# Optimization experiments

Hardware: AMD Instinct MI355X
Metric: run time of the kernel (lower is better)

The kernel has to match this reference:

```python
import jax, jax.numpy as jnp
import numpy as np
import math

B, T, D, H, E = 4, 2048, 1024, 4096, 8
CAPACITY_FACTOR = 1.0
MIN_CAPACITY = 4
Z_LOSS_COEF = 0.001
AUX_LOSS_COEF = 0.01


def setup_inputs() -> dict:
    key = jax.random.key(0)
    ks = jax.random.split(key, 5)
    x = jax.random.normal(ks[0], (B, T, D), jnp.float32)
    Wg = jax.random.normal(ks[1], (D, E), jnp.float32) * 0.02
    W1 = jax.random.normal(ks[2], (E, D, H), jnp.float32) * (1.0 / math.sqrt(D))
    b1 = jnp.zeros((E, H), jnp.float32)
    W2 = jax.random.normal(ks[3], (E, H, D), jnp.float32) * (1.0 / math.sqrt(H))
    b2 = jnp.zeros((E, D), jnp.float32)
    return {"x": x, "Wg": Wg, "W1": W1, "b1": b1, "W2": W2, "b2": b2}


def reference(x, Wg, W1, b1, W2, b2):
    b, t, d = x.shape
    e = Wg.shape[1]
    N = b * t
    capacity = max(MIN_CAPACITY, math.ceil(CAPACITY_FACTOR * N / e))  # static
    xf = x.reshape(N, d)

    # ---- Router (top-1, z-loss + aux load-balancing loss) ----
    logits = xf @ Wg                                   # [N, E]
    probs = jax.nn.softmax(logits, axis=-1)
    z_loss = jnp.mean(jax.nn.logsumexp(logits, axis=-1) ** 2)
    expert_index = jnp.argmax(logits, axis=-1)         # [N]
    expert_prob = jnp.take_along_axis(probs, expert_index[:, None], axis=1)[:, 0]
    counts = jax.ops.segment_sum(jnp.ones((N,), jnp.float32), expert_index,
                                 num_segments=e)       # bincount
    f_i = counts / N
    p_i = probs.mean(axis=0)
    aux_loss = AUX_LOSS_COEF * e * jnp.sum(f_i * p_i) + Z_LOSS_COEF * z_loss

    # ---- Sort-based dispatch ----
    sort_idx = jnp.argsort(expert_index)               # stable sort by expert
    se = expert_index[sort_idx]                        # sorted expert ids
    xs = xf[sort_idx]                                  # tokens in sorted order
    ps = expert_prob[sort_idx]                         # probs in sorted order
    counts_i = counts.astype(jnp.int32)
    start = jnp.cumsum(counts_i) - counts_i            # per-expert start offsets
    pos = jnp.arange(N, dtype=jnp.int32) - start[se]   # slot within expert
    keep = pos < capacity                              # capacity drop
    slot = jnp.where(keep, pos, capacity)              # overflow -> trash slot

    # Gather tokens into per-expert capacity buffer [E, capacity+1, D]
    buf = jnp.zeros((e, capacity + 1, d), xf.dtype).at[se, slot].set(xs)

    # ---- Batched per-expert MLP (grouped GEMM) ----
    h = jax.nn.gelu(jnp.einsum('ecd,edh->ech', buf, W1) + b1[:, None, :],
                    approximate=False)
    o = jnp.einsum('ech,ehd->ecd', h, W2) + b2[:, None, :]

    # ---- Combine: gather back, zero dropped tokens, unsort ----
    out_sorted = jnp.where(keep[:, None], o[se, slot], jnp.zeros((), o.dtype))
    out = jnp.zeros_like(xf).at[sort_idx].set(out_sorted)
    # NOTE: faithful to original code, which multiplies the UNSORTED output by
    # the SORTED probabilities (prob_sorted), a quirk of the source module.
    out = out * ps[:, None]
    return out.reshape(b, t, d), aux_loss
```

## Files before the change

kernel.cpp:

```cpp
#include <hip/hip_runtime.h>
#include <math.h>

#define N_TOK 8192
#define DIM   1024
#define NEXP  8
#define HID   4096
#define CAP   1024
#define TPT   (N_TOK / 256)
#define RT_BLOCKS 1024
#define RT_TPB 8

typedef _Float16 f16x8 __attribute__((ext_vector_type(8)));
typedef _Float16 f16x4 __attribute__((ext_vector_type(4)));
typedef float    f32x4 __attribute__((ext_vector_type(4)));

__device__ __forceinline__ float gelu_fast(float v) {
    const float v2 = v * v;
    const float u = v * (0.79788456f + 0.035677408136f * v2);
    const float ex = __expf(2.f * u);
    const float th = 1.f - 2.f / (1.f + ex);
    return 0.5f * v * (1.f + th);
}

__device__ __forceinline__ void gl_lds16(const void* g, void* l) {
    __builtin_amdgcn_global_load_lds(
        (const __attribute__((address_space(1))) unsigned int*)g,
        (__attribute__((address_space(3))) unsigned int*)l, 16, 0, 0);
}

__global__ __launch_bounds__(256) void router_kernel(
    const float* __restrict__ x, const float* __restrict__ Wg,
    int* __restrict__ ei, float* __restrict__ eprob,
    float* __restrict__ pp)
{
    __shared__ float psum_s[NEXP + 1];
    const int tid = threadIdx.x;
    const int w = tid >> 6, lane = tid & 63;
    if (tid <= NEXP) psum_s[tid] = 0.f;
    __syncthreads();

    float p_loc[NEXP];
#pragma unroll
    for (int e = 0; e < NEXP; ++e) p_loc[e] = 0.f;
    float z_loc = 0.f;

#pragma unroll
    for (int ti = 0; ti < 2; ++ti) {
        const int t = blockIdx.x * RT_TPB + w * 2 + ti;
        const float* xr = x + (size_t)t * DIM;
        float acc[NEXP];
#pragma unroll
        for (int e = 0; e < NEXP; ++e) acc[e] = 0.f;
#pragma unroll
        for (int k = 0; k < DIM / 256; ++k) {
            const int d = k * 256 + lane * 4;
            const float4 xv = *(const float4*)(xr + d);
            const float xs[4] = {xv.x, xv.y, xv.z, xv.w};
#pragma unroll
            for (int u = 0; u < 4; ++u) {
                const float4 w0 = *(const float4*)(Wg + (size_t)(d + u) * NEXP);
                const float4 w1 = *(const float4*)(Wg + (size_t)(d + u) * NEXP + 4);
                acc[0] += xs[u] * w0.x; acc[1] += xs[u] * w0.y;
                acc[2] += xs[u] * w0.z; acc[3] += xs[u] * w0.w;
                acc[4] += xs[u] * w1.x; acc[5] += xs[u] * w1.y;
                acc[6] += xs[u] * w1.z; acc[7] += xs[u] * w1.w;
            }
        }
#pragma unroll
        for (int off = 32; off > 0; off >>= 1) {
#pragma unroll
            for (int e = 0; e < NEXP; ++e)
                acc[e] += __shfl_down(acc[e], off, 64);
        }
        if (lane == 0) {
            float m = acc[0]; int arg = 0;
#pragma unroll
            for (int e = 1; e < NEXP; ++e) { if (acc[e] > m) { m = acc[e]; arg = e; } }
            float ex[NEXP]; float se = 0.f;
#pragma unroll
            for (int e = 0; e < NEXP; ++e) { ex[e] = expf(acc[e] - m); se += ex[e]; }
            const float lse = m + logf(se);
            const float inv = 1.f / se;
#pragma unroll
            for (int e = 0; e < NEXP; ++e) p_loc[e] += ex[e] * inv;
            z_loc += lse * lse;
            ei[t] = arg;
            eprob[t] = ex[arg] * inv;
        }
    }
    if (lane == 0) {
#pragma unroll
        for (int e = 0; e < NEXP; ++e) atomicAdd(&psum_s[e], p_loc[e]);
        atomicAdd(&psum_s[NEXP], z_loc);
    }
    __syncthreads();
    if (tid <= NEXP) pp[blockIdx.x * (NEXP + 1) + tid] = psum_s[tid];
}

__global__ __launch_bounds__(256) void dispatch_kernel(
    const int* __restrict__ ei, const float* __restrict__ eprob,
    int* __restrict__ slot_to_token, int* __restrict__ sort_idx,
    float* __restrict__ scale,
    const float* __restrict__ pp,
    int* __restrict__ dropped, int* __restrict__ n_dropped,
    float* __restrict__ aux_out)
{
    __shared__ int hist[NEXP][256];
    __shared__ int start_s[NEXP];
    __shared__ float red_s[4][NEXP + 1];
    __shared__ float tot_s[NEXP + 1];
    __shared__ int ndrop_s;
    const int t = threadIdx.x;
    const int w = t >> 6, lane = t & 63;
    if (t == 0) ndrop_s = 0;

    {
        float v[NEXP + 1];
#pragma unroll
        for (int j = 0; j <= NEXP; ++j) v[j] = 0.f;
        for (int g = 0; g < RT_BLOCKS / 256; ++g)
#pragma unroll
            for (int j = 0; j <= NEXP; ++j) v[j] += pp[(size_t)(g * 256 + t) * (NEXP + 1) + j];
#pragma unroll
        for (int j = 0; j <= NEXP; ++j) {
            float s = v[j];
#pragma unroll
            for (int off = 32; off > 0; off >>= 1) s += __shfl_down(s, off, 64);
            if (lane == 0) red_s[w][j] = s;
        }
    }
    __syncthreads();
    if (t <= NEXP) tot_s[t] = red_s[0][t] + red_s[1][t] + red_s[2][t] + red_s[3][t];
    __syncthreads();

    int le[TPT];
    int lh[NEXP];
#pragma unroll
    for (int e = 0; e < NEXP; ++e) lh[e] = 0;
    const int base = t * TPT;
    for (int i = 0; i < TPT; ++i) {
        const int e = ei[base + i];
        le[i] = e;
        lh[e]++;
    }
#pragma unroll
    for (int e = 0; e < NEXP; ++e) hist[e][t] = lh[e];
    __syncthreads();
    for (int off = 1; off < 256; off <<= 1) {
        int v[NEXP];
#pragma unroll
        for (int e = 0; e < NEXP; ++e) v[e] = (t >= off) ? hist[e][t - off] : 0;
        __syncthreads();
#pragma unroll
        for (int e = 0; e < NEXP; ++e) hist[e][t] += v[e];
        __syncthreads();
    }
    if (t == 0) {
        int s = 0;
        for (int e = 0; e < NEXP; ++e) { start_s[e] = s; s += hist[e][255]; }
    }
    __syncthreads();
    int run[NEXP];
#pragma unroll
    for (int e = 0; e < NEXP; ++e) run[e] = (t > 0) ? hist[e][t - 1] : 0;
    for (int i = 0; i < TPT; ++i) {
        const int n = base + i;
        const int e = le[i];
        const int pos = run[e]++;
        sort_idx[start_s[e] + pos] = n;
        if (pos < CAP) {
            slot_to_token[e * CAP + pos] = n;
        } else {
            const int di = atomicAdd(&ndrop_s, 1);
            dropped[di] = n;
        }
    }
    __syncthreads();
    for (int n = t; n < N_TOK; n += 256) scale[n] = eprob[sort_idx[n]];
    if (t == 0) {
        n_dropped[0] = ndrop_s;
        float s = 0.f;
        for (int e = 0; e < NEXP; ++e) {
            const float f = (float)hist[e][255] / (float)N_TOK;
            const float p = tot_s[e] / (float)N_TOK;
            s += f * p;
        }
        aux_out[0] = 0.01f * (float)NEXP * s + 0.001f * (tot_s[NEXP] / (float)N_TOK);
    }
}

__global__ __launch_bounds__(256) void zero_dropped_kernel(
    const int* __restrict__ dropped, const int* __restrict__ n_dropped,
    float* __restrict__ out)
{
    const int nd = n_dropped[0];
    const float4 z = make_float4(0.f, 0.f, 0.f, 0.f);
    for (int idx = blockIdx.x; idx < nd; idx += gridDim.x) {
        const int tok = dropped[idx];
        *(float4*)(out + (size_t)tok * DIM + threadIdx.x * 4) = z;
    }
}

__global__ __launch_bounds__(256) void gather_kernel(
    const float* __restrict__ x, const int* __restrict__ slot_to_token,
    _Float16* __restrict__ Xbuf)
{
    const int slot = blockIdx.x;
    const int tok = slot_to_token[slot];
    const int c = threadIdx.x * 4;
    float4 v = make_float4(0.f, 0.f, 0.f, 0.f);
    if (tok >= 0) v = *(const float4*)(x + (size_t)tok * DIM + c);
    f16x4 o;
    o[0] = (_Float16)v.x; o[1] = (_Float16)v.y;
    o[2] = (_Float16)v.z; o[3] = (_Float16)v.w;
    *(f16x4*)(Xbuf + (size_t)slot * DIM + c) = o;
}

template<int R, int C>
__global__ __launch_bounds__(256) void transpose_f32_f16(
    const float* __restrict__ in, _Float16* __restrict__ outT)
{
    const int e = blockIdx.z;
    const int r0 = blockIdx.y * 64, c0 = blockIdx.x * 64;
    const float* pin = in + (size_t)e * R * C;
    _Float16* pot = outT + (size_t)e * R * C;
    __shared__ _Float16 tile[64][72];
    const int tid = threadIdx.x;
    const int rr = tid >> 4, cc = (tid & 15) * 4;
#pragma unroll
    for (int ri = 0; ri < 4; ++ri) {
        const int row = rr + ri * 16;
        const float4 v = *(const float4*)&pin[(size_t)(r0 + row) * C + c0 + cc];
        tile[cc + 0][row] = (_Float16)v.x;
        tile[cc + 1][row] = (_Float16)v.y;
        tile[cc + 2][row] = (_Float16)v.z;
        tile[cc + 3][row] = (_Float16)v.w;
    }
    __syncthreads();
    const int c = tid >> 2, rs = (tid & 3) * 16;
    const f16x8 o0 = *(const f16x8*)&tile[c][rs];
    const f16x8 o1 = *(const f16x8*)&tile[c][rs + 8];
    _Float16* po = &pot[(size_t)(c0 + c) * R + r0 + rs];
    *(f16x8*)po = o0;
    *(f16x8*)(po + 8) = o1;
}

__global__ __launch_bounds__(256) void gemm1_kernel(
    const _Float16* __restrict__ A, const _Float16* __restrict__ Bt,
    const float* __restrict__ b1, _Float16* __restrict__ Hbuf)
{
    const int b = blockIdx.x;
    const int xcd = b & 7, q = b >> 3;
    const int nb = (xcd << 2) | (q & 3);
    const int mb = q >> 2;
    const int e  = mb >> 3;
    const _Float16* Ab = A  + (size_t)mb * 128 * DIM;
    const _Float16* Bb = Bt + (size_t)e * HID * DIM + (size_t)nb * 128 * DIM;
    __shared__ _Float16 As[128 * 64];
    __shared__ _Float16 Bs[128 * 64];
    const int tid = threadIdx.x;
    const int lane = tid & 63, w = tid >> 6;
    const int wm = (w >> 1) * 64, wn = (w & 1) * 64;
    const int lr = lane & 15, quad = lane >> 4;

    f32x4 acc[4][4];
#pragma unroll
    for (int i = 0; i < 4; ++i)
#pragma unroll
        for (int j = 0; j < 4; ++j) acc[i][j] = (f32x4)0.f;

    for (int k0 = 0; k0 < DIM; k0 += 64) {
#pragma unroll
        for (int i = 0; i < 4; ++i) {
            const int idx = i * 256 + tid;
            const int row = idx >> 3, s = idx & 7;
            const int seg = s ^ (row & 7);
            gl_lds16(Ab + (size_t)row * DIM + k0 + seg * 8, &As[idx * 8]);
            gl_lds16(Bb + (size_t)row * DIM + k0 + seg * 8, &Bs[idx * 8]);
        }
        __syncthreads();
#pragma unroll
        for (int kk = 0; kk < 2; ++kk) {
            f16x8 af[4], bf[4];
#pragma unroll
            for (int i = 0; i < 4; ++i) {
                const int R = wm + i * 16 + lr;
                af[i] = *(const f16x8*)&As[R * 64 + (((kk << 2) | quad) ^ (R & 7)) * 8];
            }
#pragma unroll
            for (int j = 0; j < 4; ++j) {
                const int R = wn + j * 16 + lr;
                bf[j] = *(const f16x8*)&Bs[R * 64 + (((kk << 2) | quad) ^ (R & 7)) * 8];
            }
#pragma unroll
            for (int i = 0; i < 4; ++i)
#pragma unroll
                for (int j = 0; j < 4; ++j)
                    acc[i][j] = __builtin_amdgcn_mfma_f32_16x16x32_f16(af[i], bf[j], acc[i][j], 0, 0, 0);
        }
        __syncthreads();
    }
    float bias[4];
#pragma unroll
    for (int j = 0; j < 4; ++j)
        bias[j] = b1[(size_t)e * HID + (size_t)nb * 128 + wn + j * 16 + lr];
#pragma unroll
    for (int i = 0; i < 4; ++i) {
#pragma unroll
        for (int r = 0; r < 4; ++r) {
            const size_t row = (size_t)mb * 128 + wm + i * 16 + quad * 4 + r;
            _Float16* hr = Hbuf + row * HID + (size_t)nb * 128;
#pragma unroll
            for (int j = 0; j < 4; ++j)
                hr[wn + j * 16 + lr] = (_Float16)gelu_fast(acc[i][j][r] + bias[j]);
        }
    }
}

__global__ __launch_bounds__(256) void gemm2_kernel(
    const _Float16* __restrict__ A, const _Float16* __restrict__ Bt,
    const float* __restrict__ b2, const int* __restrict__ slot_to_token,
    const float* __restrict__ scale, float* __restrict__ out)
{
    const int b = blockIdx.x;
    const int xcd = b & 7, q = b >> 3;
    const int nb = (xcd << 1) | (q & 1);
    const int mb = q >> 1;
    const int e  = mb >> 3;
    const _Float16* Ab = A  + (size_t)mb * 128 * HID;
    const _Float16* Bb = Bt + (size_t)e * DIM * HID + (size_t)nb * 64 * HID;
    __shared__ _Float16 As[128 * 64];
    __shared__ _Float16 Bs[64 * 64];
    const int tid = threadIdx.x;
    const int lane = tid & 63, w = tid >> 6;
    const int wm = (w >> 1) * 64, wn = (w & 1) * 32;
    const int lr = lane & 15, quad = lane >> 4;

    f32x4 acc[4][2];
#pragma unroll
    for (int i = 0; i < 4; ++i)
#pragma unroll
        for (int j = 0; j < 2; ++j) acc[i][j] = (f32x4)0.f;

    for (int k0 = 0; k0 < HID; k0 += 64) {
#pragma unroll
        for (int i = 0; i < 4; ++i) {
            const int idx = i * 256 + tid;
            const int row = idx >> 3, s = idx & 7;
            const int seg = s ^ (row & 7);
            gl_lds16(Ab + (size_t)row * HID + k0 + seg * 8, &As[idx * 8]);
        }
#pragma unroll
        for (int i = 0; i < 2; ++i) {
            const int idx = i * 256 + tid;
            const int row = idx >> 3, s = idx & 7;
            const int seg = s ^ (row & 7);
            gl_lds16(Bb + (size_t)row * HID + k0 + seg * 8, &Bs[idx * 8]);
        }
        __syncthreads();
#pragma unroll
        for (int kk = 0; kk < 2; ++kk) {
            f16x8 af[4], bf[2];
#pragma unroll
            for (int i = 0; i < 4; ++i) {
                const int R = wm + i * 16 + lr;
                af[i] = *(const f16x8*)&As[R * 64 + (((kk << 2) | quad) ^ (R & 7)) * 8];
            }
#pragma unroll
            for (int j = 0; j < 2; ++j) {
                const int R = wn + j * 16 + lr;
                bf[j] = *(const f16x8*)&Bs[R * 64 + (((kk << 2) | quad) ^ (R & 7)) * 8];
            }
#pragma unroll
            for (int i = 0; i < 4; ++i)
#pragma unroll
                for (int j = 0; j < 2; ++j)
                    acc[i][j] = __builtin_amdgcn_mfma_f32_16x16x32_f16(af[i], bf[j], acc[i][j], 0, 0, 0);
        }
        __syncthreads();
    }
    float bias[2];
#pragma unroll
    for (int j = 0; j < 2; ++j)
        bias[j] = b2[(size_t)e * DIM + (size_t)nb * 64 + wn + j * 16 + lr];
#pragma unroll
    for (int i = 0; i < 4; ++i) {
#pragma unroll
        for (int r = 0; r < 4; ++r) {
            const int slot = mb * 128 + wm + i * 16 + quad * 4 + r;
            const int tok = slot_to_token[slot];
            if (tok >= 0) {
                const float sc = scale[tok];
                float* orow = out + (size_t)tok * DIM + (size_t)nb * 64;
#pragma unroll
                for (int j = 0; j < 2; ++j)
                    orow[wn + j * 16 + lr] = (acc[i][j][r] + bias[j]) * sc;
            }
        }
    }
}

extern "C" void kernel_launch(void* const* d_in, const int* in_sizes, int n_in,
                              void* d_out, int out_size, void* d_ws, size_t ws_size,
                              hipStream_t stream)
{
    const float* x  = (const float*)d_in[0];
    const float* Wg = (const float*)d_in[1];
    const float* W1 = (const float*)d_in[2];
    const float* b1 = (const float*)d_in[3];
    const float* W2 = (const float*)d_in[4];
    const float* b2 = (const float*)d_in[5];
    float* out = (float*)d_out;

    _Float16* Wt   = (_Float16*)d_ws;
    _Float16* Xbuf = Wt + (size_t)NEXP * HID * DIM;
    _Float16* Hbuf = Xbuf + (size_t)N_TOK * DIM;
    int*   ei    = (int*)(Hbuf + (size_t)N_TOK * HID);
    float* eprob = (float*)(ei + N_TOK);
    int*   sort_idx = (int*)(eprob + N_TOK);
    float* scale = (float*)(sort_idx + N_TOK);
    int*   s2t   = (int*)(scale + N_TOK);
    float* pp    = (float*)(s2t + NEXP * CAP);
    int*   dropped = (int*)(pp + RT_BLOCKS * (NEXP + 1));
    int*   n_dropped = dropped + N_TOK;

    hipMemsetAsync(s2t, 0xFF, (size_t)NEXP * CAP * sizeof(int), stream);

    transpose_f32_f16<DIM, HID><<<dim3(HID / 64, DIM / 64, NEXP), 256, 0, stream>>>(W1, Wt);
    router_kernel<<<RT_BLOCKS, 256, 0, stream>>>(x, Wg, ei, eprob, pp);
    dispatch_kernel<<<1, 256, 0, stream>>>(ei, eprob, s2t, sort_idx, scale,
                                           pp, dropped, n_dropped,
                                           out + (size_t)N_TOK * DIM);
    zero_dropped_kernel<<<128, 256, 0, stream>>>(dropped, n_dropped, out);
    gather_kernel<<<NEXP * CAP, 256, 0, stream>>>(x, s2t, Xbuf);
    gemm1_kernel<<<2048, 256, 0, stream>>>(Xbuf, Wt, b1, Hbuf);
    transpose_f32_f16<HID, DIM><<<dim3(DIM / 64, HID / 64, NEXP), 256, 0, stream>>>(W2, Wt);
    gemm2_kernel<<<1024, 256, 0, stream>>>(Hbuf, Wt, b2, s2t, scale, out);
}
```

Measured before the change: 597.7 us.

## Double-buffer expert GEMMs with 256-row tiles, 512-thread blocks and XCD-aligned experts

Both grouped GEMM kernels move to 512-thread blocks with larger tiles: 256x256 for the first GEMM and 256x128 for the second. Each uses double-buffered LDS so the next K-tile loads while MFMAs run on the current one, split into four phases with raised wave priority around the MFMA bursts. Blocks are mapped so each XCD handles one expert's weights, which should improve L2 reuse of the weight tiles. The larger LDS footprint and register use reduce occupancy, and the grid shrinks to 512 and 256 blocks, which may leave tail imbalance across CUs.

```diff
diff --git a/kernel.cpp b/kernel.cpp
--- a/kernel.cpp
+++ b/kernel.cpp
@@ -245,156 +245,217 @@
     *(f16x8*)(po + 8) = o1;
 }
 
-__global__ __launch_bounds__(256) void gemm1_kernel(
+
+__global__ __launch_bounds__(512, 2) void gemm1_kernel(
     const _Float16* __restrict__ A, const _Float16* __restrict__ Bt,
     const float* __restrict__ b1, _Float16* __restrict__ Hbuf)
 {
     const int b = blockIdx.x;
     const int xcd = b & 7, q = b >> 3;
-    const int nb = (xcd << 2) | (q & 3);
-    const int mb = q >> 2;
-    const int e  = mb >> 3;
-    const _Float16* Ab = A  + (size_t)mb * 128 * DIM;
-    const _Float16* Bb = Bt + (size_t)e * HID * DIM + (size_t)nb * 128 * DIM;
-    __shared__ _Float16 As[128 * 64];
-    __shared__ _Float16 Bs[128 * 64];
+    const int mb = (xcd << 2) | (q & 3);
+    const int nb = q >> 2;
+    const int e  = xcd;
+    const _Float16* Ab = A  + (size_t)mb * 256 * DIM;
+    const _Float16* Bb = Bt + (size_t)e * HID * DIM + (size_t)nb * 256 * DIM;
+    __shared__ _Float16 As[2][256 * 64];
+    __shared__ _Float16 Bs[2][256 * 64];
     const int tid = threadIdx.x;
     const int lane = tid & 63, w = tid >> 6;
-    const int wm = (w >> 1) * 64, wn = (w & 1) * 64;
+    const int wr = w >> 2, wc = w & 3;
     const int lr = lane & 15, quad = lane >> 4;
-
-    f32x4 acc[4][4];
-#pragma unroll
-    for (int i = 0; i < 4; ++i)
-#pragma unroll
-        for (int j = 0; j < 4; ++j) acc[i][j] = (f32x4)0.f;
-
-    for (int k0 = 0; k0 < DIM; k0 += 64) {
+    const int rb = wr * 128, cb = wc * 64;
+
+    auto stageA = [&](int t, int buf) {
 #pragma unroll
         for (int i = 0; i < 4; ++i) {
-            const int idx = i * 256 + tid;
+            const int idx = i * 512 + tid;
             const int row = idx >> 3, s = idx & 7;
             const int seg = s ^ (row & 7);
-            gl_lds16(Ab + (size_t)row * DIM + k0 + seg * 8, &As[idx * 8]);
-            gl_lds16(Bb + (size_t)row * DIM + k0 + seg * 8, &Bs[idx * 8]);
-        }
-        __syncthreads();
-#pragma unroll
-        for (int kk = 0; kk < 2; ++kk) {
-            f16x8 af[4], bf[4];
-#pragma unroll
-            for (int i = 0; i < 4; ++i) {
-                const int R = wm + i * 16 + lr;
-                af[i] = *(const f16x8*)&As[R * 64 + (((kk << 2) | quad) ^ (R & 7)) * 8];
-            }
-#pragma unroll
-            for (int j = 0; j < 4; ++j) {
-                const int R = wn + j * 16 + lr;
-                bf[j] = *(const f16x8*)&Bs[R * 64 + (((kk << 2) | quad) ^ (R & 7)) * 8];
-            }
-#pragma unroll
-            for (int i = 0; i < 4; ++i)
-#pragma unroll
-                for (int j = 0; j < 4; ++j)
-                    acc[i][j] = __builtin_amdgcn_mfma_f32_16x16x32_f16(af[i], bf[j], acc[i][j], 0, 0, 0);
-        }
-        __syncthreads();
-    }
+            gl_lds16(Ab + (size_t)row * DIM + t * 64 + seg * 8, &As[buf][idx * 8]);
+        }
+    };
+    auto stageB = [&](int t, int buf) {
+#pragma unroll
+        for (int i = 0; i < 4; ++i) {
+            const int idx = i * 512 + tid;
+            const int row = idx >> 3, s = idx & 7;
+            const int seg = s ^ (row & 7);
+            gl_lds16(Bb + (size_t)row * DIM + t * 64 + seg * 8, &Bs[buf][idx * 8]);
+        }
+    };
+
+    f32x4 acc[8][4];
+#pragma unroll
+    for (int i = 0; i < 8; ++i)
+#pragma unroll
+        for (int j = 0; j < 4; ++j) acc[i][j] = (f32x4)0.f;
+
+    stageA(0, 0);
+    stageB(0, 0);
+    const int NT = DIM / 64;
+#pragma unroll 2
+    for (int t = 0; t < NT; ++t) {
+        const int cur = t & 1, nxt = cur ^ 1;
+        asm volatile("s_waitcnt vmcnt(0)" ::: "memory");
+        __builtin_amdgcn_s_barrier();
+#pragma unroll
+        for (int ph = 0; ph < 4; ++ph) {
+            if (ph == 0 && t + 1 < NT) stageA(t + 1, nxt);
+            if (ph == 1 && t + 1 < NT) stageB(t + 1, nxt);
+            const int mih = (ph >> 1) * 4, njh = (ph & 1) * 2;
+            f16x8 af[4][2], bf[2][2];
+#pragma unroll
+            for (int mi = 0; mi < 4; ++mi)
+#pragma unroll
+                for (int kk = 0; kk < 2; ++kk) {
+                    const int R = rb + (mih + mi) * 16 + lr;
+                    af[mi][kk] = *(const f16x8*)&As[cur][R * 64 + (((kk << 2) | quad) ^ (R & 7)) * 8];
+                }
+#pragma unroll
+            for (int nj = 0; nj < 2; ++nj)
+#pragma unroll
+                for (int kk = 0; kk < 2; ++kk) {
+                    const int R = cb + (njh + nj) * 16 + lr;
+                    bf[nj][kk] = *(const f16x8*)&Bs[cur][R * 64 + (((kk << 2) | quad) ^ (R & 7)) * 8];
+                }
+            __builtin_amdgcn_s_barrier();
+            __builtin_amdgcn_s_setprio(1);
+#pragma unroll
+            for (int kk = 0; kk < 2; ++kk)
+#pragma unroll
+                for (int mi = 0; mi < 4; ++mi)
+#pragma unroll
+                    for (int nj = 0; nj < 2; ++nj)
+                        acc[mih + mi][njh + nj] = __builtin_amdgcn_mfma_f32_16x16x32_f16(
+                            af[mi][kk], bf[nj][kk], acc[mih + mi][njh + nj], 0, 0, 0);
+            __builtin_amdgcn_s_setprio(0);
+            if (ph < 3) __builtin_amdgcn_s_barrier();
+        }
+    }
+
+    const int colb = nb * 256 + cb;
     float bias[4];
 #pragma unroll
-    for (int j = 0; j < 4; ++j)
-        bias[j] = b1[(size_t)e * HID + (size_t)nb * 128 + wn + j * 16 + lr];
-#pragma unroll
-    for (int i = 0; i < 4; ++i) {
+    for (int nj = 0; nj < 4; ++nj)
+        bias[nj] = b1[(size_t)e * HID + colb + nj * 16 + lr];
+#pragma unroll
+    for (int mi = 0; mi < 8; ++mi) {
 #pragma unroll
         for (int r = 0; r < 4; ++r) {
-            const size_t row = (size_t)mb * 128 + wm + i * 16 + quad * 4 + r;
-            _Float16* hr = Hbuf + row * HID + (size_t)nb * 128;
-#pragma unroll
-            for (int j = 0; j < 4; ++j)
-                hr[wn + j * 16 + lr] = (_Float16)gelu_fast(acc[i][j][r] + bias[j]);
-        }
-    }
-}
-
-__global__ __launch_bounds__(256) void gemm2_kernel(
+            const size_t row = (size_t)mb * 256 + rb + mi * 16 + quad * 4 + r;
+            _Float16* hr = Hbuf + row * HID + colb;
+#pragma unroll
+            for (int nj = 0; nj < 4; ++nj)
+                hr[nj * 16 + lr] = (_Float16)gelu_fast(acc[mi][nj][r] + bias[nj]);
+        }
+    }
+}
+
+__global__ __launch_bounds__(512, 2) void gemm2_kernel(
     const _Float16* __restrict__ A, const _Float16* __restrict__ Bt,
     const float* __restrict__ b2, const int* __restrict__ slot_to_token,
     const float* __restrict__ scale, float* __restrict__ out)
 {
     const int b = blockIdx.x;
     const int xcd = b & 7, q = b >> 3;
-    const int nb = (xcd << 1) | (q & 1);
-    const int mb = q >> 1;
-    const int e  = mb >> 3;
-    const _Float16* Ab = A  + (size_t)mb * 128 * HID;
-    const _Float16* Bb = Bt + (size_t)e * DIM * HID + (size_t)nb * 64 * HID;
-    __shared__ _Float16 As[128 * 64];
-    __shared__ _Float16 Bs[64 * 64];
+    const int mb = (xcd << 2) | (q & 3);
+    const int nb = q >> 2;
+    const int e  = xcd;
+    const _Float16* Ab = A  + (size_t)mb * 256 * HID;
+    const _Float16* Bb = Bt + (size_t)e * DIM * HID + (size_t)nb * 128 * HID;
+    __shared__ _Float16 As[2][256 * 64];
+    __shared__ _Float16 Bs[2][128 * 64];
     const int tid = threadIdx.x;
     const int lane = tid & 63, w = tid >> 6;
-    const int wm = (w >> 1) * 64, wn = (w & 1) * 32;
+    const int wr = w >> 1, wc = w & 1;
     const int lr = lane & 15, quad = lane >> 4;
-
-    f32x4 acc[4][2];
-#pragma unroll
-    for (int i = 0; i < 4; ++i)
-#pragma unroll
-        for (int j = 0; j < 2; ++j) acc[i][j] = (f32x4)0.f;
-
-    for (int k0 = 0; k0 < HID; k0 += 64) {
+    const int rb = wr * 64, cb = wc * 64;
+
+    auto stageA = [&](int t, int buf) {
 #pragma unroll
         for (int i = 0; i < 4; ++i) {
-            const int idx = i * 256 + tid;
+            const int idx = i * 512 + tid;
             const int row = idx >> 3, s = idx & 7;
             const int seg = s ^ (row & 7);
-            gl_lds16(Ab + (size_t)row * HID + k0 + seg * 8, &As[idx * 8]);
-        }
+            gl_lds16(Ab + (size_t)row * HID + t * 64 + seg * 8, &As[buf][idx * 8]);
+        }
+    };
+    auto stageB = [&](int t, int buf) {
 #pragma unroll
         for (int i = 0; i < 2; ++i) {
-            const int idx = i * 256 + tid;
+            const int idx = i * 512 + tid;
             const int row = idx >> 3, s = idx & 7;
             const int seg = s ^ (row & 7);
-            gl_lds16(Bb + (size_t)row * HID + k0 + seg * 8, &Bs[idx * 8]);
-        }
-        __syncthreads();
-#pragma unroll
-        for (int kk = 0; kk < 2; ++kk) {
-            f16x8 af[4], bf[2];
-#pragma unroll
-            for (int i = 0; i < 4; ++i) {
-                const int R = wm + i * 16 + lr;
-                af[i] = *(const f16x8*)&As[R * 64 + (((kk << 2) | quad) ^ (R & 7)) * 8];
-            }
-#pragma unroll
-            for (int j = 0; j < 2; ++j) {
-                const int R = wn + j * 16 + lr;
-                bf[j] = *(const f16x8*)&Bs[R * 64 + (((kk << 2) | quad) ^ (R & 7)) * 8];
-            }
-#pragma unroll
-            for (int i = 0; i < 4; ++i)
-#pragma unroll
-                for (int j = 0; j < 2; ++j)
-                    acc[i][j] = __builtin_amdgcn_mfma_f32_16x16x32_f16(af[i], bf[j], acc[i][j], 0, 0, 0);
-        }
-        __syncthreads();
-    }
-    float bias[2];
-#pragma unroll
-    for (int j = 0; j < 2; ++j)
-        bias[j] = b2[(size_t)e * DIM + (size_t)nb * 64 + wn + j * 16 + lr];
-#pragma unroll
-    for (int i = 0; i < 4; ++i) {
+            gl_lds16(Bb + (size_t)row * HID + t * 64 + seg * 8, &Bs[buf][idx * 8]);
+        }
+    };
+
+    f32x4 acc[4][4];
+#pragma unroll
+    for (int i = 0; i < 4; ++i)
+#pragma unroll
+        for (int j = 0; j < 4; ++j) acc[i][j] = (f32x4)0.f;
+
+    stageA(0, 0);
+    stageB(0, 0);
+    const int NT = HID / 64;
+#pragma unroll 2
+    for (int t = 0; t < NT; ++t) {
+        const int cur = t & 1, nxt = cur ^ 1;
+        asm volatile("s_waitcnt vmcnt(0)" ::: "memory");
+        __builtin_amdgcn_s_barrier();
+#pragma unroll
+        for (int ph = 0; ph < 4; ++ph) {
+            if (ph == 0 && t + 1 < NT) stageA(t + 1, nxt);
+            if (ph == 1 && t + 1 < NT) stageB(t + 1, nxt);
+            const int mih = (ph >> 1) * 2, njh = (ph & 1) * 2;
+            f16x8 af[2][2], bf[2][2];
+#pragma unroll
+            for (int mi = 0; mi < 2; ++mi)
+#pragma unroll
+                for (int kk = 0; kk < 2; ++kk) {
+                    const int R = rb + (mih + mi) * 16 + lr;
+                    af[mi][kk] = *(const f16x8*)&As[cur][R * 64 + (((kk << 2) | quad) ^ (R & 7)) * 8];
+                }
+#pragma unroll
+            for (int nj = 0; nj < 2; ++nj)
+#pragma unroll
+                for (int kk = 0; kk < 2; ++kk) {
+                    const int R = cb + (njh + nj) * 16 + lr;
+                    bf[nj][kk] = *(const f16x8*)&Bs[cur][R * 64 + (((kk << 2) | quad) ^ (R & 7)) * 8];
+                }
+            __builtin_amdgcn_s_barrier();
+            __builtin_amdgcn_s_setprio(1);
+#pragma unroll
+            for (int kk = 0; kk < 2; ++kk)
+#pragma unroll
+                for (int mi = 0; mi < 2; ++mi)
+#pragma unroll
+                    for (int nj = 0; nj < 2; ++nj)
+                        acc[mih + mi][njh + nj] = __builtin_amdgcn_mfma_f32_16x16x32_f16(
+                            af[mi][kk], bf[nj][kk], acc[mih + mi][njh + nj], 0, 0, 0);
+            __builtin_amdgcn_s_setprio(0);
+            if (ph < 3) __builtin_amdgcn_s_barrier();
+        }
+    }
+
+    const int colb = nb * 128 + cb;
+    float bias[4];
+#pragma unroll
+    for (int nj = 0; nj < 4; ++nj)
+        bias[nj] = b2[(size_t)e * DIM + colb + nj * 16 + lr];
+#pragma unroll
+    for (int mi = 0; mi < 4; ++mi) {
 #pragma unroll
         for (int r = 0; r < 4; ++r) {
-            const int slot = mb * 128 + wm + i * 16 + quad * 4 + r;
+            const int slot = mb * 256 + rb + mi * 16 + quad * 4 + r;
             const int tok = slot_to_token[slot];
             if (tok >= 0) {
                 const float sc = scale[tok];
-                float* orow = out + (size_t)tok * DIM + (size_t)nb * 64;
-#pragma unroll
-                for (int j = 0; j < 2; ++j)
-                    orow[wn + j * 16 + lr] = (acc[i][j][r] + bias[j]) * sc;
+                float* orow = out + (size_t)tok * DIM + colb;
+#pragma unroll
+                for (int nj = 0; nj < 4; ++nj)
+                    orow[nj * 16 + lr] = (acc[mi][nj][r] + bias[nj]) * sc;
             }
         }
     }
@@ -433,7 +494,7 @@
                                            out + (size_t)N_TOK * DIM);
     zero_dropped_kernel<<<128, 256, 0, stream>>>(dropped, n_dropped, out);
     gather_kernel<<<NEXP * CAP, 256, 0, stream>>>(x, s2t, Xbuf);
-    gemm1_kernel<<<2048, 256, 0, stream>>>(Xbuf, Wt, b1, Hbuf);
+    gemm1_kernel<<<512, 512, 0, stream>>>(Xbuf, Wt, b1, Hbuf);
     transpose_f32_f16<HID, DIM><<<dim3(DIM / 64, HID / 64, NEXP), 256, 0, stream>>>(W2, Wt);
-    gemm2_kernel<<<1024, 256, 0, stream>>>(Hbuf, Wt, b2, s2t, scale, out);
-}
+    gemm2_kernel<<<256, 512, 0, stream>>>(Hbuf, Wt, b2, s2t, scale, out);
+}
```

Measured after the change: 592.0 us. About the same (-0.9%).
